# Kernel optimization log

Measured on AMD Instinct MI355X. Metric: run time of the kernel, lower is better.

## Reference

```python
import jax, jax.numpy as jnp
import numpy as np

R = 256        # residual channels
SKIP = 256     # skip channels
COND = 80      # conditioning (mel) channels
NUM_CLS = 256  # mu-law classes
T = 1024       # samples to generate
DILATIONS = tuple([1, 2, 4, 8, 16, 32, 64, 128, 256, 512] * 3)  # 30 layers, kernel_size=2
L = len(DILATIONS)


def setup_inputs() -> dict:
    key = jax.random.key(0)
    ks = jax.random.split(key, 15)
    sc = 0.05
    f = jnp.float32
    return {
        "y": jax.random.normal(ks[0], (COND, T), f),
        "emb": jnp.tanh(jax.random.normal(ks[1], (NUM_CLS, R), f)),  # buffer stores emb.tanh()
        "condition_W": jax.random.normal(ks[2], (L * 2 * R, COND), f) * sc,
        "WV_past": jax.random.normal(ks[3], (L, 2 * R, R), f) * sc,      # K=2 -> one past tap
        "WV_present": jax.random.normal(ks[4], (L, 2 * R, R), f) * sc,
        "W_o_weight": jax.random.normal(ks[5], (L - 1, R + SKIP, R), f) * sc,
        "W_o_bias": jax.random.normal(ks[6], (L - 1, R + SKIP), f) * sc,
        "W_o_weight_last": jax.random.normal(ks[7], (SKIP, R), f) * sc,
        "W_o_bias_last": jax.random.normal(ks[8], (SKIP,), f) * sc,
        "end1_w": jax.random.normal(ks[9], (SKIP, SKIP), f) * sc,
        "end1_b": jax.random.normal(ks[10], (SKIP,), f) * sc,
        "end2_w": jax.random.normal(ks[11], (NUM_CLS, SKIP), f) * sc,
        "end2_b": jax.random.normal(ks[12], (NUM_CLS,), f) * sc,
        "samples": jax.random.uniform(ks[13], (T,), f),  # torch.rand(T) inverse-CDF draws
    }


def _generate(y, emb, condition_W, WV_past, WV_present, W_o_weight, W_o_bias,
              W_o_weight_last, W_o_bias_last, end1_w, end1_b, end2_w, end2_b,
              samples, c=1.0):
    # all conditioning projections at once; chunked per layer as in torch.chunk(.., L, dim=0)
    conds_seq = (condition_W @ y).T.reshape(T, L, 2 * R)  # [T, L, 2R]
    x0 = emb[NUM_CLS // 2 - 1]
    mems0 = tuple(jnp.zeros((R, d), y.dtype) for d in DILATIONS)  # ring buffers per layer
    idx0 = jnp.zeros((L,), jnp.int32)

    def step(carry, inp):
        mems, idxs, x = carry
        cond_t, u = inp
        skip = jnp.zeros((SKIP,), x.dtype)
        new_mems, new_idxs = [], []
        for j in range(L):  # fixed small layer loop (structurally distinct buffers)
            mem, idx = mems[j], idxs[j]
            # kernel_size=2 -> single past tap read from ring buffer at idx
            h = cond_t[j] + WV_past[j] @ jnp.take(mem, idx, axis=1) + WV_present[j] @ x
            mem = mem.at[:, idx].set(x)  # write present sample, advance ring pointer
            new_mems.append(mem)
            new_idxs.append((idx + 1) % mem.shape[1])
            zw, zf = jnp.split(h, 2)
            z = jnp.tanh(zw) * jax.nn.sigmoid(zf)  # gated activation
            if j < L - 1:
                z2 = W_o_weight[j] @ z + W_o_bias[j]
                x = x + z2[:R]          # residual
                skip = skip + z2[R:]    # skip accumulation
            else:
                skip = skip + W_o_weight_last @ z + W_o_bias_last
        hid = jax.nn.relu(end1_w @ jax.nn.relu(skip) + end1_b)
        logits = (end2_w @ hid + end2_b) * c
        cum = jnp.cumsum(jax.nn.softmax(logits))
        new_idx = jnp.argmax(cum > u)  # first index with cum-prob > u  (inverse-CDF sample)
        return (tuple(new_mems), jnp.stack(new_idxs), emb[new_idx]), (new_idx, logits)

    _, (outputs, logits) = jax.lax.scan(step, (mems0, idx0, x0), (conds_seq, samples))
    return outputs.astype(jnp.int64), logits


def reference(y, emb, condition_W, WV_past, WV_present, W_o_weight, W_o_bias,
              W_o_weight_last, W_o_bias_last, end1_w, end1_b, end2_w, end2_b, samples):
    outputs, _ = _generate(y, emb, condition_W, WV_past, WV_present, W_o_weight,
                           W_o_bias, W_o_weight_last, W_o_bias_last,
                           end1_w, end1_b, end2_w, end2_b, samples)
    return outputs
```

## Files before the change

kernel.cpp:

```cpp
#include <hip/hip_runtime.h>
#include <stdint.h>


typedef unsigned long long u64;

#define TT 1024

#define OFF_PG   0
#define OFF_PS   (OFF_PG + 30*8*256*8)
#define OFF_XV   (OFF_PS + 30*8*256*8)
#define OFF_SB   (OFF_XV + 30*256*8)
#define OFF_HID  (OFF_SB + 30*256*8)
#define OFF_IDX  (OFF_HID + 256*8)
#define OFF_XH   (OFF_IDX + 64)
#define WS_NEED  ((size_t)OFF_XH + (size_t)30*1024*256*4)

__device__ __forceinline__ u64 ldp(const u64* p){
    return __hip_atomic_load((u64*)p, __ATOMIC_RELAXED, __HIP_MEMORY_SCOPE_AGENT);
}
__device__ __forceinline__ void stp(u64* p, float v, unsigned stamp){
    union { float f; unsigned u; } c; c.f = v;
    u64 w = ((u64)stamp << 32) | (u64)c.u;
    __hip_atomic_store(p, w, __ATOMIC_RELAXED, __HIP_MEMORY_SCOPE_AGENT);
}
__device__ __forceinline__ void stpu(u64* p, unsigned v, unsigned stamp){
    u64 w = ((u64)stamp << 32) | (u64)v;
    __hip_atomic_store(p, w, __ATOMIC_RELAXED, __HIP_MEMORY_SCOPE_AGENT);
}
__device__ __forceinline__ float pf(u64 w){
    union { unsigned u; float f; } c; c.u = (unsigned)(w & 0xffffffffu); return c.f;
}
__device__ __forceinline__ unsigned pstamp(u64 w){ return (unsigned)(w >> 32); }
__device__ __forceinline__ float ldf(const float* p){
    return __hip_atomic_load((float*)p, __ATOMIC_RELAXED, __HIP_MEMORY_SCOPE_AGENT);
}
__device__ __forceinline__ void stf(float* p, float v){
    __hip_atomic_store(p, v, __ATOMIC_RELAXED, __HIP_MEMORY_SCOPE_AGENT);
}
__device__ __forceinline__ long long rt(){
    return (long long)__builtin_amdgcn_s_memrealtime();
}
__device__ __forceinline__ void bar_lds(){
    asm volatile("s_waitcnt lgkmcnt(0)\n\ts_barrier" ::: "memory");
}

__global__ void __launch_bounds__(256, 1)
wavenet_v2(const float* __restrict__ gy,   const float* __restrict__ gemb,
           const float* __restrict__ gcw,  const float* __restrict__ gwvp,
           const float* __restrict__ gwvx, const float* __restrict__ gwo,
           const float* __restrict__ gwob, const float* __restrict__ gwol,
           const float* __restrict__ gwobl,const float* __restrict__ ge1w,
           const float* __restrict__ ge1b, const float* __restrict__ ge2w,
           const float* __restrict__ ge2b, const float* __restrict__ gsmp,
           float one, int* __restrict__ gout, char* __restrict__ ws)
{
    const int b = blockIdx.x, tid = threadIdx.x;
    const int xcd = b & 7, kk = b >> 3;
    const int jj = 4*xcd + (kk >> 3);
    const int cc = kk & 7;

    if (jj > 30 || (jj == 30 && cc > 2)) return;

    u64* PG   = (u64*)(ws + OFF_PG);
    u64* PS   = (u64*)(ws + OFF_PS);
    u64* XV   = (u64*)(ws + OFF_XV);
    u64* SB   = (u64*)(ws + OFF_SB);
    u64* HIDP = (u64*)(ws + OFF_HID);
    u64* IDXP = (u64*)(ws + OFF_IDX);
    float* xh = (float*)(ws + OFF_XH);

    __shared__ float sTap[256];
    __shared__ float sXin[256];
    __shared__ float sY[80];
    __shared__ float sZ[32];
    __shared__ float sred[8];
    __shared__ int   sidx[4];

    const long long ddl = rt() + 400000000LL;

    if (jj < 30){
        const int j   = jj;
        const int dil = 1 << (j % 10);
        const int q   = tid & 3;
        const int s   = (tid >> 2) & 15;
        const int w   = tid >> 6;
        const int gr  = (s < 8) ? (32*cc + 8*w + s)
                                : (256 + 32*cc + 8*w + (s - 8));

        const float* rw = (q < 2) ? (gwvp + ((size_t)j*512 + gr)*256 + 128*q)
                                  : (gwvx + ((size_t)j*512 + gr)*256 + 128*(q-2));
        float wv[128];
        #pragma unroll
        for (int i = 0; i < 32; i++){
            const int ci = (i + 2*q) & 31;
            wv[4*i+0] = rw[4*ci+0]*one; wv[4*i+1] = rw[4*ci+1]*one;
            wv[4*i+2] = rw[4*ci+2]*one; wv[4*i+3] = rw[4*ci+3]*one;
        }
        float cw[20];
        {
            const float* cp = gcw + ((size_t)(j*512 + gr))*80 + 20*q;
            #pragma unroll
            for (int i = 0; i < 20; i++) cw[i] = cp[i]*one;
        }
        float wo2[64]; float bres = 0.f, bskip = 0.f;
        if (j < 29){
            const float* w0 = gwo + ((size_t)j*512 + tid)*256 + 32*cc;
            const float* w1 = gwo + ((size_t)j*512 + 256 + tid)*256 + 32*cc;
            #pragma unroll
            for (int i = 0; i < 32; i++){ wo2[i] = w0[i]*one; wo2[32+i] = w1[i]*one; }
            bres  = gwob[j*512 + tid];
            bskip = gwob[j*512 + 256 + tid];
        } else {
            const float* w0 = gwol + (size_t)tid*256 + 32*cc;
            #pragma unroll
            for (int i = 0; i < 32; i++){ wo2[i] = w0[i]*one; wo2[32+i] = 0.f; }
            bskip = gwobl[tid];
        }

        u64* pgj = PG + (size_t)j*8*256;
        u64* psj = PS + (size_t)j*8*256;
        const u64* pgp = PG + (size_t)(j > 0 ? j-1 : 0)*8*256 + tid;
        const u64* psp = PS + (size_t)(j > 0 ? j-1 : 0)*8*256 + tid;
        const u64* xvp = XV + (size_t)(j > 0 ? j-1 : 0)*256 + tid;
        const u64* sbp = SB + (size_t)(j >= 2 ? j-1 : 0)*256 + tid;
        float* xhj = xh + (size_t)j*1024*256;
        float xv_prev = 0.f;

        for (int t = 0; t < TT; t++){
            const unsigned stamp = (unsigned)(t + 1);

            if (tid < 80) sY[tid] = gy[tid*TT + t];
            float tapv;
            if (dil == 1) tapv = xv_prev;
            else          tapv = (t >= dil) ? ldf(xhj + (size_t)(t-dil)*256 + tid) : 0.f;
            sTap[tid] = tapv;
            bar_lds();

            float acc = 0.f;
            #pragma unroll
            for (int i = 0; i < 20; i++) acc = fmaf(cw[i], sY[20*q + i], acc);
            if (q < 2){
                const float4* x4 = (const float4*)(sTap + 128*q);
                #pragma unroll
                for (int i = 0; i < 32; i++){
                    const int ci = (i + 2*q) & 31;
                    float4 v = x4[ci];
                    acc = fmaf(wv[4*i+0], v.x, acc); acc = fmaf(wv[4*i+1], v.y, acc);
                    acc = fmaf(wv[4*i+2], v.z, acc); acc = fmaf(wv[4*i+3], v.w, acc);
                }
            }

            float xv;
            if (j == 0){
                if (t == 0){
                    xv = gemb[127*256 + tid];
                } else {
                    u64 wIdx; int c = 0;
                    do {
                        wIdx = ldp(IDXP);
                        if (((++c) & 255) == 0 && rt() > ddl) break;
                    } while (pstamp(wIdx) != (unsigned)t);
                    const int idx = (int)(wIdx & 0xffffffffu) & 255;
                    xv = gemb[idx*256 + tid];
                }
            } else {
                u64 gwv[8]; u64 xvw = 0; u64 swv[8]; u64 sbw = 0;
                bool fresh; int c = 0;
                do {
                    #pragma unroll
                    for (int c2 = 0; c2 < 8; c2++) gwv[c2] = ldp(pgp + c2*256);
                    xvw = ldp(xvp);
                    bool ok = (pstamp(xvw) == stamp);
                    #pragma unroll
                    for (int c2 = 0; c2 < 8; c2++) ok &= (pstamp(gwv[c2]) == stamp);
                    if (cc == 0){
                        #pragma unroll
                        for (int c2 = 0; c2 < 8; c2++){
                            swv[c2] = ldp(psp + c2*256);
                            ok &= (pstamp(swv[c2]) == stamp);
                        }
                        if (j >= 2){ sbw = ldp(sbp); ok &= (pstamp(sbw) == stamp); }
                    }
                    fresh = ok;
                    if (((++c) & 255) == 0 && rt() > ddl) break;
                } while (!fresh);
                xv = pf(xvw);
                #pragma unroll
                for (int c2 = 0; c2 < 8; c2++) xv += pf(gwv[c2]);
                if (cc == 0){
                    float sv = (j >= 2) ? pf(sbw) : 0.f;
                    #pragma unroll
                    for (int c2 = 0; c2 < 8; c2++) sv += pf(swv[c2]);
                    stp(SB + (size_t)j*256 + tid, sv, stamp);
                }
            }
            xv_prev = xv;
            sXin[tid] = xv;
            if (cc == 0){
                stp(XV + (size_t)j*256 + tid, xv, stamp);
                if (dil > 1) stf(xhj + (size_t)t*256 + tid, xv);
            }
            bar_lds();

            if (q >= 2){
                const float4* x4 = (const float4*)(sXin + 128*(q-2));
                #pragma unroll
                for (int i = 0; i < 32; i++){
                    const int ci = (i + 2*q) & 31;
                    float4 v = x4[ci];
                    acc = fmaf(wv[4*i+0], v.x, acc); acc = fmaf(wv[4*i+1], v.y, acc);
                    acc = fmaf(wv[4*i+2], v.z, acc); acc = fmaf(wv[4*i+3], v.w, acc);
                }
            }
            acc += __shfl_xor(acc, 1, 64);
            acc += __shfl_xor(acc, 2, 64);
            const float hpart = __shfl_xor(acc, 32, 64);
            if (q == 0 && s < 8)
                sZ[8*w + s] = tanhf(acc) * (1.f/(1.f + expf(-hpart)));
            bar_lds();

            float g = 0.f, sk = 0.f;
            const float4* z4 = (const float4*)sZ;
            #pragma unroll
            for (int i = 0; i < 8; i++){
                float4 v = z4[i];
                g  = fmaf(wo2[4*i+0], v.x, g);  g  = fmaf(wo2[4*i+1], v.y, g);
                g  = fmaf(wo2[4*i+2], v.z, g);  g  = fmaf(wo2[4*i+3], v.w, g);
                sk = fmaf(wo2[32+4*i+0], v.x, sk); sk = fmaf(wo2[32+4*i+1], v.y, sk);
                sk = fmaf(wo2[32+4*i+2], v.z, sk); sk = fmaf(wo2[32+4*i+3], v.w, sk);
            }
            if (j < 29){
                if (cc == 0){ g += bres; sk += bskip; }
                stp(pgj + cc*256 + tid, g,  stamp);
                stp(psj + cc*256 + tid, sk, stamp);
            } else {
                if (cc == 0) g += bskip;
                stp(psj + cc*256 + tid, g, stamp);
            }
        }
        return;
    }

    if (jj == 30 && cc < 2){
        const int half = cc;
        const int r  = 128*half + (tid >> 1);
        const int hc = tid & 1;
        float e1[128];
        {
            const float* wp = ge1w + (size_t)r*256 + 128*hc;
            #pragma unroll
            for (int i = 0; i < 128; i++) e1[i] = wp[i]*one;
        }
        const float b1 = ge1b[r];
        const u64* psp = PS + (size_t)29*8*256 + tid;
        const u64* sbp = SB + (size_t)29*256 + tid;

        for (int t = 0; t < TT; t++){
            const unsigned stamp = (unsigned)(t + 1);
            u64 swv[8]; u64 sbw = 0; bool fresh; int c = 0;
            do {
                #pragma unroll
                for (int c2 = 0; c2 < 8; c2++) swv[c2] = ldp(psp + c2*256);
                sbw = ldp(sbp);
                bool ok = (pstamp(sbw) == stamp);
                #pragma unroll
                for (int c2 = 0; c2 < 8; c2++) ok &= (pstamp(swv[c2]) == stamp);
                fresh = ok;
                if (((++c) & 255) == 0 && rt() > ddl) break;
            } while (!fresh);
            float sk = pf(sbw);
            #pragma unroll
            for (int c2 = 0; c2 < 8; c2++) sk += pf(swv[c2]);
            sTap[tid] = fmaxf(sk, 0.f);
            bar_lds();
            float a = 0.f;
            const float4* p4 = (const float4*)(sTap + 128*hc);
            #pragma unroll
            for (int i = 0; i < 32; i++){
                float4 v = p4[i];
                a = fmaf(e1[4*i+0], v.x, a); a = fmaf(e1[4*i+1], v.y, a);
                a = fmaf(e1[4*i+2], v.z, a); a = fmaf(e1[4*i+3], v.w, a);
            }
            a += __shfl_xor(a, 1, 64);
            if (hc == 0) stp(HIDP + r, fmaxf(a + b1, 0.f), stamp);
            bar_lds();
        }
        return;
    }

    {
        float e2[256];
        {
            const float* wp = ge2w + (size_t)tid*256;
            #pragma unroll
            for (int i = 0; i < 256; i++) e2[i] = wp[i]*one;
        }
        const float b2 = ge2b[tid];
        const int w = tid >> 6, lane = tid & 63;

        for (int t = 0; t < TT; t++){
            const unsigned stamp = (unsigned)(t + 1);
            u64 hw; int c = 0;
            do {
                hw = ldp(HIDP + tid);
                if (((++c) & 255) == 0 && rt() > ddl) break;
            } while (pstamp(hw) != stamp);
            sTap[tid] = pf(hw);
            bar_lds();
            float a = b2;
            const float4* p4 = (const float4*)sTap;
            #pragma unroll
            for (int i = 0; i < 64; i++){
                float4 v = p4[i];
                a = fmaf(e2[4*i+0], v.x, a); a = fmaf(e2[4*i+1], v.y, a);
                a = fmaf(e2[4*i+2], v.z, a); a = fmaf(e2[4*i+3], v.w, a);
            }
            float m = a;
            #pragma unroll
            for (int off = 32; off > 0; off >>= 1) m = fmaxf(m, __shfl_xor(m, off, 64));
            if (lane == 0) sred[w] = m;
            bar_lds();
            m = fmaxf(fmaxf(sred[0], sred[1]), fmaxf(sred[2], sred[3]));
            float pe = expf(a - m);
            float ssum = pe;
            #pragma unroll
            for (int off = 32; off > 0; off >>= 1) ssum += __shfl_xor(ssum, off, 64);
            if (lane == 0) sred[4 + w] = ssum;
            bar_lds();
            const float S = sred[4] + sred[5] + sred[6] + sred[7];
            float cum = pe / S;
            #pragma unroll
            for (int off = 1; off < 64; off <<= 1){
                float vv = __shfl_up(cum, off, 64);
                if (lane >= off) cum += vv;
            }
            if (lane == 63) sred[w] = cum;
            bar_lds();
            float base = 0.f;
            if (w > 0) base += sred[0];
            if (w > 1) base += sred[1];
            if (w > 2) base += sred[2];
            cum += base;
            const float u = gsmp[t];
            unsigned long long bal = __ballot(cum > u);
            int cand = bal ? (w*64 + __ffsll((long long)bal) - 1) : (1 << 30);
            if (lane == 0) sidx[w] = cand;
            bar_lds();
            int idx = min(min(sidx[0], sidx[1]), min(sidx[2], sidx[3]));
            if (idx > 255) idx = 0;
            if (tid == 0){
                gout[t] = idx;
                stpu(IDXP, (unsigned)idx, stamp);
            }
            bar_lds();
        }
        return;
    }
}

__global__ void ws_too_small_kernel(int* out, int n){
    int i = blockIdx.x*256 + threadIdx.x;
    if (i < n) out[i] = 0;
}

extern "C" void kernel_launch(void* const* d_in, const int* in_sizes, int n_in,
                              void* d_out, int out_size, void* d_ws, size_t ws_size,
                              hipStream_t stream){
    (void)in_sizes; (void)n_in;
    if (ws_size < WS_NEED){
        hipLaunchKernelGGL(ws_too_small_kernel, dim3(4), dim3(256), 0, stream,
                           (int*)d_out, out_size);
        return;
    }
    hipLaunchKernelGGL(wavenet_v2, dim3(256), dim3(256), 0, stream,
                       (const float*)d_in[0],  (const float*)d_in[1],
                       (const float*)d_in[2],  (const float*)d_in[3],
                       (const float*)d_in[4],  (const float*)d_in[5],
                       (const float*)d_in[6],  (const float*)d_in[7],
                       (const float*)d_in[8],  (const float*)d_in[9],
                       (const float*)d_in[10], (const float*)d_in[11],
                       (const float*)d_in[12], (const float*)d_in[13],
                       1.0f, (int*)d_out, (char*)d_ws);
}
```

Before: 108.5 ms.

## Pack inter-layer flag records contiguously and move skip reduction to head block

Replaces the scattered per-chunk stamped buffers with one contiguous 128-byte record per layer row, holding the 8 gate partials plus xv, so a consumer polls it with five vector loads. The per-layer skip-sum chain through cc==0 blocks is removed. Skip partials go into a per-row array that the end1 block polls and sums directly over 30 layers. It also uses inline asm loads/stores with sc0 sc1 cache bypass and keeps weights in vector registers. This shortens the critical dependency chain between layers, at the cost of more polling work in the head block.

Result: slower. 195.2 ms (+79.8%).

```diff
diff --git a/kernel.cpp b/kernel.cpp
--- a/kernel.cpp
+++ b/kernel.cpp
@@ -3,68 +3,115 @@
 
 
 typedef unsigned long long u64;
+typedef float v16 __attribute__((ext_vector_type(16)));
 
 #define TT 1024
 
-#define OFF_PG   0
-#define OFF_PS   (OFF_PG + 30*8*256*8)
-#define OFF_XV   (OFF_PS + 30*8*256*8)
-#define OFF_SB   (OFF_XV + 30*256*8)
-#define OFF_HID  (OFF_SB + 30*256*8)
+#define OFF_REC  4096
+#define OFF_SPR  (OFF_REC + 29*256*128)
+#define OFF_HID  (OFF_SPR + 256*256*8)
 #define OFF_IDX  (OFF_HID + 256*8)
 #define OFF_XH   (OFF_IDX + 64)
 #define WS_NEED  ((size_t)OFF_XH + (size_t)30*1024*256*4)
 
-__device__ __forceinline__ u64 ldp(const u64* p){
-    return __hip_atomic_load((u64*)p, __ATOMIC_RELAXED, __HIP_MEMORY_SCOPE_AGENT);
-}
-__device__ __forceinline__ void stp(u64* p, float v, unsigned stamp){
+__device__ __forceinline__ long long rt(){
+    return (long long)__builtin_amdgcn_s_memrealtime();
+}
+__device__ __forceinline__ u64 pk(unsigned stamp, float v){
     union { float f; unsigned u; } c; c.f = v;
-    u64 w = ((u64)stamp << 32) | (u64)c.u;
-    __hip_atomic_store(p, w, __ATOMIC_RELAXED, __HIP_MEMORY_SCOPE_AGENT);
-}
-__device__ __forceinline__ void stpu(u64* p, unsigned v, unsigned stamp){
-    u64 w = ((u64)stamp << 32) | (u64)v;
-    __hip_atomic_store(p, w, __ATOMIC_RELAXED, __HIP_MEMORY_SCOPE_AGENT);
-}
-__device__ __forceinline__ float pf(u64 w){
-    union { unsigned u; float f; } c; c.u = (unsigned)(w & 0xffffffffu); return c.f;
-}
-__device__ __forceinline__ unsigned pstamp(u64 w){ return (unsigned)(w >> 32); }
+    return ((u64)stamp << 32) | (u64)c.u;
+}
+__device__ __forceinline__ u64 pku(unsigned stamp, unsigned v){
+    return ((u64)stamp << 32) | (u64)v;
+}
+__device__ __forceinline__ float uaf(unsigned u){
+    union { unsigned u; float f; } c; c.u = u; return c.f;
+}
+__device__ __forceinline__ unsigned pst(u64 w){ return (unsigned)(w >> 32); }
 __device__ __forceinline__ float ldf(const float* p){
     return __hip_atomic_load((float*)p, __ATOMIC_RELAXED, __HIP_MEMORY_SCOPE_AGENT);
 }
 __device__ __forceinline__ void stf(float* p, float v){
     __hip_atomic_store(p, v, __ATOMIC_RELAXED, __HIP_MEMORY_SCOPE_AGENT);
 }
-__device__ __forceinline__ long long rt(){
-    return (long long)__builtin_amdgcn_s_memrealtime();
+
+__device__ __forceinline__ u64 ld8_s(const void* p){
+    u64 r;
+    asm volatile("global_load_dwordx2 %0, %1, off sc0 sc1\n\ts_waitcnt vmcnt(0)"
+                 : "=&v"(r) : "v"(p) : "memory");
+    return r;
+}
+__device__ __forceinline__ void st8_s(void* p, u64 v){
+    asm volatile("global_store_dwordx2 %0, %1, off sc0 sc1" :: "v"(p), "v"(v) : "memory");
+}
+__device__ __forceinline__ void poll5_s(const void* p, uint4& a, uint4& b, uint4& c,
+                                        uint4& d, uint4& e){
+    asm volatile(
+        "global_load_dwordx4 %0, %5, off sc0 sc1\n\t"
+        "global_load_dwordx4 %1, %5, off offset:16 sc0 sc1\n\t"
+        "global_load_dwordx4 %2, %5, off offset:32 sc0 sc1\n\t"
+        "global_load_dwordx4 %3, %5, off offset:48 sc0 sc1\n\t"
+        "global_load_dwordx4 %4, %5, off offset:64 sc0 sc1\n\t"
+        "s_waitcnt vmcnt(0)"
+        : "=&v"(a),"=&v"(b),"=&v"(c),"=&v"(d),"=&v"(e) : "v"(p) : "memory");
+}
+__device__ __forceinline__ void poll4_s(const void* p, uint4& a, uint4& b, uint4& c,
+                                        uint4& d){
+    asm volatile(
+        "global_load_dwordx4 %0, %4, off sc0 sc1\n\t"
+        "global_load_dwordx4 %1, %4, off offset:16 sc0 sc1\n\t"
+        "global_load_dwordx4 %2, %4, off offset:32 sc0 sc1\n\t"
+        "global_load_dwordx4 %3, %4, off offset:48 sc0 sc1\n\t"
+        "s_waitcnt vmcnt(0)"
+        : "=&v"(a),"=&v"(b),"=&v"(c),"=&v"(d) : "v"(p) : "memory");
 }
 __device__ __forceinline__ void bar_lds(){
     asm volatile("s_waitcnt lgkmcnt(0)\n\ts_barrier" ::: "memory");
 }
 
+#define LD16(W, P) { \
+  W[0]=(P)[0]*one;  W[1]=(P)[1]*one;  W[2]=(P)[2]*one;  W[3]=(P)[3]*one;  \
+  W[4]=(P)[4]*one;  W[5]=(P)[5]*one;  W[6]=(P)[6]*one;  W[7]=(P)[7]*one;  \
+  W[8]=(P)[8]*one;  W[9]=(P)[9]*one;  W[10]=(P)[10]*one;W[11]=(P)[11]*one;\
+  W[12]=(P)[12]*one;W[13]=(P)[13]*one;W[14]=(P)[14]*one;W[15]=(P)[15]*one;\
+}
+
+#define MAT16(W, X4, C, ACC) { \
+  { float4 v_=(X4)[4*(C)+0]; ACC=fmaf(W[0],v_.x,ACC);  ACC=fmaf(W[1],v_.y,ACC);  ACC=fmaf(W[2],v_.z,ACC);  ACC=fmaf(W[3],v_.w,ACC); } \
+  { float4 v_=(X4)[4*(C)+1]; ACC=fmaf(W[4],v_.x,ACC);  ACC=fmaf(W[5],v_.y,ACC);  ACC=fmaf(W[6],v_.z,ACC);  ACC=fmaf(W[7],v_.w,ACC); } \
+  { float4 v_=(X4)[4*(C)+2]; ACC=fmaf(W[8],v_.x,ACC);  ACC=fmaf(W[9],v_.y,ACC);  ACC=fmaf(W[10],v_.z,ACC); ACC=fmaf(W[11],v_.w,ACC);} \
+  { float4 v_=(X4)[4*(C)+3]; ACC=fmaf(W[12],v_.x,ACC); ACC=fmaf(W[13],v_.y,ACC); ACC=fmaf(W[14],v_.z,ACC); ACC=fmaf(W[15],v_.w,ACC);} \
+}
+
+#define LDWV1(W, I, E) { const float* p_ = rw + 4*(((I)+twoq)&31); \
+  W[E+0]=p_[0]*one; W[E+1]=p_[1]*one; W[E+2]=p_[2]*one; W[E+3]=p_[3]*one; }
+#define LDWV(W, K) LDWV1(W,4*(K)+0,0) LDWV1(W,4*(K)+1,4) LDWV1(W,4*(K)+2,8) LDWV1(W,4*(K)+3,12)
+#define MATWV1(W, I, E, X4) { float4 v_=(X4)[(((I)+twoq)&31)]; \
+  acc=fmaf(W[E+0],v_.x,acc); acc=fmaf(W[E+1],v_.y,acc); acc=fmaf(W[E+2],v_.z,acc); acc=fmaf(W[E+3],v_.w,acc); }
+#define MATWV(W, K, X4) MATWV1(W,4*(K)+0,0,X4) MATWV1(W,4*(K)+1,4,X4) MATWV1(W,4*(K)+2,8,X4) MATWV1(W,4*(K)+3,12,X4)
+
+#define MATZ1(W, I, E, ACC) { float4 v_=z4[(I)]; \
+  ACC=fmaf(W[E+0],v_.x,ACC); ACC=fmaf(W[E+1],v_.y,ACC); ACC=fmaf(W[E+2],v_.z,ACC); ACC=fmaf(W[E+3],v_.w,ACC); }
+#define MATZ(W, IB, ACC) MATZ1(W,(IB)+0,0,ACC) MATZ1(W,(IB)+1,4,ACC) MATZ1(W,(IB)+2,8,ACC) MATZ1(W,(IB)+3,12,ACC)
+
 __global__ void __launch_bounds__(256, 1)
-wavenet_v2(const float* __restrict__ gy,   const float* __restrict__ gemb,
-           const float* __restrict__ gcw,  const float* __restrict__ gwvp,
-           const float* __restrict__ gwvx, const float* __restrict__ gwo,
-           const float* __restrict__ gwob, const float* __restrict__ gwol,
-           const float* __restrict__ gwobl,const float* __restrict__ ge1w,
-           const float* __restrict__ ge1b, const float* __restrict__ ge2w,
-           const float* __restrict__ ge2b, const float* __restrict__ gsmp,
-           float one, int* __restrict__ gout, char* __restrict__ ws)
+wavenet_v3c(const float* __restrict__ gy,   const float* __restrict__ gemb,
+            const float* __restrict__ gcw,  const float* __restrict__ gwvp,
+            const float* __restrict__ gwvx, const float* __restrict__ gwo,
+            const float* __restrict__ gwob, const float* __restrict__ gwol,
+            const float* __restrict__ gwobl,const float* __restrict__ ge1w,
+            const float* __restrict__ ge1b, const float* __restrict__ ge2w,
+            const float* __restrict__ ge2b, const float* __restrict__ gsmp,
+            float one, int* __restrict__ gout, char* __restrict__ ws)
 {
     const int b = blockIdx.x, tid = threadIdx.x;
-    const int xcd = b & 7, kk = b >> 3;
-    const int jj = 4*xcd + (kk >> 3);
+    const int xcdh = b & 7, kk = b >> 3;
+    const int jj = 4*xcdh + (kk >> 3);
     const int cc = kk & 7;
-
     if (jj > 30 || (jj == 30 && cc > 2)) return;
 
-    u64* PG   = (u64*)(ws + OFF_PG);
-    u64* PS   = (u64*)(ws + OFF_PS);
-    u64* XV   = (u64*)(ws + OFF_XV);
-    u64* SB   = (u64*)(ws + OFF_SB);
+    u64* REC  = (u64*)(ws + OFF_REC);
+    u64* SPR  = (u64*)(ws + OFF_SPR);
     u64* HIDP = (u64*)(ws + OFF_HID);
     u64* IDXP = (u64*)(ws + OFF_IDX);
     float* xh = (float*)(ws + OFF_XH);
@@ -84,45 +131,39 @@
         const int q   = tid & 3;
         const int s   = (tid >> 2) & 15;
         const int w   = tid >> 6;
-        const int gr  = (s < 8) ? (32*cc + 8*w + s)
-                                : (256 + 32*cc + 8*w + (s - 8));
+        const int twoq = 2*q;
+        const int gr  = (s < 8) ? (32*cc + 8*w + s) : (256 + 32*cc + 8*w + (s - 8));
 
         const float* rw = (q < 2) ? (gwvp + ((size_t)j*512 + gr)*256 + 128*q)
                                   : (gwvx + ((size_t)j*512 + gr)*256 + 128*(q-2));
-        float wv[128];
-        #pragma unroll
-        for (int i = 0; i < 32; i++){
-            const int ci = (i + 2*q) & 31;
-            wv[4*i+0] = rw[4*ci+0]*one; wv[4*i+1] = rw[4*ci+1]*one;
-            wv[4*i+2] = rw[4*ci+2]*one; wv[4*i+3] = rw[4*ci+3]*one;
-        }
-        float cw[20];
+        v16 wv0,wv1,wv2,wv3,wv4,wv5,wv6,wv7;
+        LDWV(wv0,0) LDWV(wv1,1) LDWV(wv2,2) LDWV(wv3,3)
+        LDWV(wv4,4) LDWV(wv5,5) LDWV(wv6,6) LDWV(wv7,7)
+
+        v16 cwa; float4 cwb;
         {
             const float* cp = gcw + ((size_t)(j*512 + gr))*80 + 20*q;
-            #pragma unroll
-            for (int i = 0; i < 20; i++) cw[i] = cp[i]*one;
-        }
-        float wo2[64]; float bres = 0.f, bskip = 0.f;
+            LD16(cwa, cp);
+            cwb.x = cp[16]*one; cwb.y = cp[17]*one; cwb.z = cp[18]*one; cwb.w = cp[19]*one;
+        }
+        const float* w0 = (j < 29) ? (gwo + ((size_t)j*512 + tid)*256 + 32*cc)
+                                   : (gwol + (size_t)tid*256 + 32*cc);
+        v16 wg0, wg1;
+        LD16(wg0, w0); LD16(wg1, w0+16);
+        v16 ws0, ws1;
+        float bres = 0.f, bskip;
         if (j < 29){
-            const float* w0 = gwo + ((size_t)j*512 + tid)*256 + 32*cc;
             const float* w1 = gwo + ((size_t)j*512 + 256 + tid)*256 + 32*cc;
-            #pragma unroll
-            for (int i = 0; i < 32; i++){ wo2[i] = w0[i]*one; wo2[32+i] = w1[i]*one; }
+            LD16(ws0, w1); LD16(ws1, w1+16);
             bres  = gwob[j*512 + tid];
             bskip = gwob[j*512 + 256 + tid];
         } else {
-            const float* w0 = gwol + (size_t)tid*256 + 32*cc;
-            #pragma unroll
-            for (int i = 0; i < 32; i++){ wo2[i] = w0[i]*one; wo2[32+i] = 0.f; }
             bskip = gwobl[tid];
         }
 
-        u64* pgj = PG + (size_t)j*8*256;
-        u64* psj = PS + (size_t)j*8*256;
-        const u64* pgp = PG + (size_t)(j > 0 ? j-1 : 0)*8*256 + tid;
-        const u64* psp = PS + (size_t)(j > 0 ? j-1 : 0)*8*256 + tid;
-        const u64* xvp = XV + (size_t)(j > 0 ? j-1 : 0)*256 + tid;
-        const u64* sbp = SB + (size_t)(j >= 2 ? j-1 : 0)*256 + tid;
+        u64* growp = REC + ((size_t)j*256 + tid)*16;
+        const char* pollb = (const char*)(REC + ((size_t)(j>0?j-1:0)*256 + tid)*16);
+        u64* sprow = SPR + (size_t)tid*256 + (size_t)j*8 + cc;
         float* xhj = xh + (size_t)j*1024*256;
         float xv_prev = 0.f;
 
@@ -137,17 +178,23 @@
             bar_lds();
 
             float acc = 0.f;
-            #pragma unroll
-            for (int i = 0; i < 20; i++) acc = fmaf(cw[i], sY[20*q + i], acc);
+            {
+                const float* yb = sY + 20*q;
+                acc=fmaf(cwa[0],yb[0],acc);   acc=fmaf(cwa[1],yb[1],acc);
+                acc=fmaf(cwa[2],yb[2],acc);   acc=fmaf(cwa[3],yb[3],acc);
+                acc=fmaf(cwa[4],yb[4],acc);   acc=fmaf(cwa[5],yb[5],acc);
+                acc=fmaf(cwa[6],yb[6],acc);   acc=fmaf(cwa[7],yb[7],acc);
+                acc=fmaf(cwa[8],yb[8],acc);   acc=fmaf(cwa[9],yb[9],acc);
+                acc=fmaf(cwa[10],yb[10],acc); acc=fmaf(cwa[11],yb[11],acc);
+                acc=fmaf(cwa[12],yb[12],acc); acc=fmaf(cwa[13],yb[13],acc);
+                acc=fmaf(cwa[14],yb[14],acc); acc=fmaf(cwa[15],yb[15],acc);
+                acc=fmaf(cwb.x,yb[16],acc);   acc=fmaf(cwb.y,yb[17],acc);
+                acc=fmaf(cwb.z,yb[18],acc);   acc=fmaf(cwb.w,yb[19],acc);
+            }
             if (q < 2){
-                const float4* x4 = (const float4*)(sTap + 128*q);
-                #pragma unroll
-                for (int i = 0; i < 32; i++){
-                    const int ci = (i + 2*q) & 31;
-                    float4 v = x4[ci];
-                    acc = fmaf(wv[4*i+0], v.x, acc); acc = fmaf(wv[4*i+1], v.y, acc);
-                    acc = fmaf(wv[4*i+2], v.z, acc); acc = fmaf(wv[4*i+3], v.w, acc);
-                }
+                const float4* x4p = (const float4*)(sTap + 128*q);
+                MATWV(wv0,0,x4p) MATWV(wv1,1,x4p) MATWV(wv2,2,x4p) MATWV(wv3,3,x4p)
+                MATWV(wv4,4,x4p) MATWV(wv5,5,x4p) MATWV(wv6,6,x4p) MATWV(wv7,7,x4p)
             }
 
             float xv;
@@ -157,60 +204,39 @@
                 } else {
                     u64 wIdx; int c = 0;
                     do {
-                        wIdx = ldp(IDXP);
+                        wIdx = ld8_s(IDXP);
                         if (((++c) & 255) == 0 && rt() > ddl) break;
-                    } while (pstamp(wIdx) != (unsigned)t);
+                    } while (pst(wIdx) != (unsigned)t);
                     const int idx = (int)(wIdx & 0xffffffffu) & 255;
                     xv = gemb[idx*256 + tid];
                 }
             } else {
-                u64 gwv[8]; u64 xvw = 0; u64 swv[8]; u64 sbw = 0;
-                bool fresh; int c = 0;
+                uint4 r0,r1,r2v,r3v,r4v; bool ok; int c = 0;
                 do {
-                    #pragma unroll
-                    for (int c2 = 0; c2 < 8; c2++) gwv[c2] = ldp(pgp + c2*256);
-                    xvw = ldp(xvp);
-                    bool ok = (pstamp(xvw) == stamp);
-                    #pragma unroll
-                    for (int c2 = 0; c2 < 8; c2++) ok &= (pstamp(gwv[c2]) == stamp);
-                    if (cc == 0){
-                        #pragma unroll
-                        for (int c2 = 0; c2 < 8; c2++){
-                            swv[c2] = ldp(psp + c2*256);
-                            ok &= (pstamp(swv[c2]) == stamp);
-                        }
-                        if (j >= 2){ sbw = ldp(sbp); ok &= (pstamp(sbw) == stamp); }
-                    }
-                    fresh = ok;
+                    poll5_s(pollb, r0,r1,r2v,r3v,r4v);
+                    ok = (r0.y==stamp) & (r0.w==stamp) & (r1.y==stamp) & (r1.w==stamp)
+                       & (r2v.y==stamp) & (r2v.w==stamp) & (r3v.y==stamp) & (r3v.w==stamp)
+                       & (r4v.y==stamp);
                     if (((++c) & 255) == 0 && rt() > ddl) break;
-                } while (!fresh);
-                xv = pf(xvw);
-                #pragma unroll
-                for (int c2 = 0; c2 < 8; c2++) xv += pf(gwv[c2]);
-                if (cc == 0){
-                    float sv = (j >= 2) ? pf(sbw) : 0.f;
-                    #pragma unroll
-                    for (int c2 = 0; c2 < 8; c2++) sv += pf(swv[c2]);
-                    stp(SB + (size_t)j*256 + tid, sv, stamp);
-                }
+                } while (!ok);
+                xv  = uaf(r4v.x);
+                xv += uaf(r0.x);  xv += uaf(r0.z);
+                xv += uaf(r1.x);  xv += uaf(r1.z);
+                xv += uaf(r2v.x); xv += uaf(r2v.z);
+                xv += uaf(r3v.x); xv += uaf(r3v.z);
             }
             xv_prev = xv;
             sXin[tid] = xv;
             if (cc == 0){
-                stp(XV + (size_t)j*256 + tid, xv, stamp);
-                if (dil > 1) stf(xhj + (size_t)t*256 + tid, xv);
+                if (j <= 28) st8_s(growp + 8, pk(stamp, xv));
+                if (dil > 1) stf(&xhj[(size_t)t*256 + tid], xv);
             }
             bar_lds();
 
             if (q >= 2){
-                const float4* x4 = (const float4*)(sXin + 128*(q-2));
-                #pragma unroll
-                for (int i = 0; i < 32; i++){
-                    const int ci = (i + 2*q) & 31;
-                    float4 v = x4[ci];
-                    acc = fmaf(wv[4*i+0], v.x, acc); acc = fmaf(wv[4*i+1], v.y, acc);
-                    acc = fmaf(wv[4*i+2], v.z, acc); acc = fmaf(wv[4*i+3], v.w, acc);
-                }
+                const float4* x4p = (const float4*)(sXin + 128*(q-2));
+                MATWV(wv0,0,x4p) MATWV(wv1,1,x4p) MATWV(wv2,2,x4p) MATWV(wv3,3,x4p)
+                MATWV(wv4,4,x4p) MATWV(wv5,5,x4p) MATWV(wv6,6,x4p) MATWV(wv7,7,x4p)
             }
             acc += __shfl_xor(acc, 1, 64);
             acc += __shfl_xor(acc, 2, 64);
@@ -219,23 +245,19 @@
                 sZ[8*w + s] = tanhf(acc) * (1.f/(1.f + expf(-hpart)));
             bar_lds();
 
-            float g = 0.f, sk = 0.f;
             const float4* z4 = (const float4*)sZ;
-            #pragma unroll
-            for (int i = 0; i < 8; i++){
-                float4 v = z4[i];
-                g  = fmaf(wo2[4*i+0], v.x, g);  g  = fmaf(wo2[4*i+1], v.y, g);
-                g  = fmaf(wo2[4*i+2], v.z, g);  g  = fmaf(wo2[4*i+3], v.w, g);
-                sk = fmaf(wo2[32+4*i+0], v.x, sk); sk = fmaf(wo2[32+4*i+1], v.y, sk);
-                sk = fmaf(wo2[32+4*i+2], v.z, sk); sk = fmaf(wo2[32+4*i+3], v.w, sk);
-            }
             if (j < 29){
+                float g = 0.f, sk = 0.f;
+                MATZ(wg0, 0, g)  MATZ(wg1, 4, g)
+                MATZ(ws0, 0, sk) MATZ(ws1, 4, sk)
                 if (cc == 0){ g += bres; sk += bskip; }
-                stp(pgj + cc*256 + tid, g,  stamp);
-                stp(psj + cc*256 + tid, sk, stamp);
+                st8_s(growp + cc, pk(stamp, g));
+                st8_s(sprow, pk(stamp, sk));
             } else {
+                float g = 0.f;
+                MATZ(wg0, 0, g) MATZ(wg1, 4, g)
                 if (cc == 0) g += bskip;
-                stp(psj + cc*256 + tid, g, stamp);
+                st8_s(sprow, pk(stamp, g));
             }
         }
         return;
@@ -245,56 +267,50 @@
         const int half = cc;
         const int r  = 128*half + (tid >> 1);
         const int hc = tid & 1;
-        float e1[128];
-        {
-            const float* wp = ge1w + (size_t)r*256 + 128*hc;
-            #pragma unroll
-            for (int i = 0; i < 128; i++) e1[i] = wp[i]*one;
-        }
+        const float* wp = ge1w + (size_t)r*256 + 128*hc;
+        v16 e0,e1v,e2v,e3,e4,e5,e6,e7;
+        LD16(e0,wp);    LD16(e1v,wp+16); LD16(e2v,wp+32); LD16(e3,wp+48);
+        LD16(e4,wp+64); LD16(e5,wp+80);  LD16(e6,wp+96);  LD16(e7,wp+112);
         const float b1 = ge1b[r];
-        const u64* psp = PS + (size_t)29*8*256 + tid;
-        const u64* sbp = SB + (size_t)29*256 + tid;
+        const u64* sprb = SPR + (size_t)tid*256;
 
         for (int t = 0; t < TT; t++){
             const unsigned stamp = (unsigned)(t + 1);
-            u64 swv[8]; u64 sbw = 0; bool fresh; int c = 0;
-            do {
-                #pragma unroll
-                for (int c2 = 0; c2 < 8; c2++) swv[c2] = ldp(psp + c2*256);
-                sbw = ldp(sbp);
-                bool ok = (pstamp(sbw) == stamp);
-                #pragma unroll
-                for (int c2 = 0; c2 < 8; c2++) ok &= (pstamp(swv[c2]) == stamp);
-                fresh = ok;
-                if (((++c) & 255) == 0 && rt() > ddl) break;
-            } while (!fresh);
-            float sk = pf(sbw);
-            #pragma unroll
-            for (int c2 = 0; c2 < 8; c2++) sk += pf(swv[c2]);
+            float sk = 0.f;
+            for (int l = 0; l < 30; l++){
+                uint4 r0,r1,r2v,r3v; bool ok; int c = 0;
+                const void* p = (const void*)(sprb + l*8);
+                do {
+                    poll4_s(p, r0,r1,r2v,r3v);
+                    ok = (r0.y==stamp)&(r0.w==stamp)&(r1.y==stamp)&(r1.w==stamp)
+                       & (r2v.y==stamp)&(r2v.w==stamp)&(r3v.y==stamp)&(r3v.w==stamp);
+                    if (((++c) & 255) == 0 && rt() > ddl) break;
+                } while (!ok);
+                sk += uaf(r0.x);  sk += uaf(r0.z);
+                sk += uaf(r1.x);  sk += uaf(r1.z);
+                sk += uaf(r2v.x); sk += uaf(r2v.z);
+                sk += uaf(r3v.x); sk += uaf(r3v.z);
+            }
             sTap[tid] = fmaxf(sk, 0.f);
             bar_lds();
             float a = 0.f;
             const float4* p4 = (const float4*)(sTap + 128*hc);
-            #pragma unroll
-            for (int i = 0; i < 32; i++){
-                float4 v = p4[i];
-                a = fmaf(e1[4*i+0], v.x, a); a = fmaf(e1[4*i+1], v.y, a);
-                a = fmaf(e1[4*i+2], v.z, a); a = fmaf(e1[4*i+3], v.w, a);
-            }
+            MAT16(e0,p4,0,a)  MAT16(e1v,p4,1,a) MAT16(e2v,p4,2,a) MAT16(e3,p4,3,a)
+            MAT16(e4,p4,4,a)  MAT16(e5,p4,5,a)  MAT16(e6,p4,6,a)  MAT16(e7,p4,7,a)
             a += __shfl_xor(a, 1, 64);
-            if (hc == 0) stp(HIDP + r, fmaxf(a + b1, 0.f), stamp);
+            if (hc == 0) st8_s(HIDP + r, pk(stamp, fmaxf(a + b1, 0.f)));
             bar_lds();
         }
         return;
     }
 
     {
-        float e2[256];
-        {
-            const float* wp = ge2w + (size_t)tid*256;
-            #pragma unroll
-            for (int i = 0; i < 256; i++) e2[i] = wp[i]*one;
-        }
+        const float* wp = ge2w + (size_t)tid*256;
+        v16 f0,f1,f2,f3,f4,f5,f6,f7,f8,f9,fa,fb,fc,fd,fe,ff;
+        LD16(f0,wp);     LD16(f1,wp+16);  LD16(f2,wp+32);  LD16(f3,wp+48);
+        LD16(f4,wp+64);  LD16(f5,wp+80);  LD16(f6,wp+96);  LD16(f7,wp+112);
+        LD16(f8,wp+128); LD16(f9,wp+144); LD16(fa,wp+160); LD16(fb,wp+176);
+        LD16(fc,wp+192); LD16(fd,wp+208); LD16(fe,wp+224); LD16(ff,wp+240);
         const float b2 = ge2b[tid];
         const int w = tid >> 6, lane = tid & 63;
 
@@ -302,19 +318,17 @@
             const unsigned stamp = (unsigned)(t + 1);
             u64 hw; int c = 0;
             do {
-                hw = ldp(HIDP + tid);
+                hw = ld8_s(HIDP + tid);
                 if (((++c) & 255) == 0 && rt() > ddl) break;
-            } while (pstamp(hw) != stamp);
-            sTap[tid] = pf(hw);
+            } while (pst(hw) != stamp);
+            sTap[tid] = uaf((unsigned)(hw & 0xffffffffu));
             bar_lds();
             float a = b2;
             const float4* p4 = (const float4*)sTap;
-            #pragma unroll
-            for (int i = 0; i < 64; i++){
-                float4 v = p4[i];
-                a = fmaf(e2[4*i+0], v.x, a); a = fmaf(e2[4*i+1], v.y, a);
-                a = fmaf(e2[4*i+2], v.z, a); a = fmaf(e2[4*i+3], v.w, a);
-            }
+            MAT16(f0,p4,0,a)  MAT16(f1,p4,1,a)  MAT16(f2,p4,2,a)  MAT16(f3,p4,3,a)
+            MAT16(f4,p4,4,a)  MAT16(f5,p4,5,a)  MAT16(f6,p4,6,a)  MAT16(f7,p4,7,a)
+            MAT16(f8,p4,8,a)  MAT16(f9,p4,9,a)  MAT16(fa,p4,10,a) MAT16(fb,p4,11,a)
+            MAT16(fc,p4,12,a) MAT16(fd,p4,13,a) MAT16(fe,p4,14,a) MAT16(ff,p4,15,a)
             float m = a;
             #pragma unroll
             for (int off = 32; off > 0; off >>= 1) m = fmaxf(m, __shfl_xor(m, off, 64));
@@ -350,7 +364,7 @@
             if (idx > 255) idx = 0;
             if (tid == 0){
                 gout[t] = idx;
-                stpu(IDXP, (unsigned)idx, stamp);
+                st8_s(IDXP, pku(stamp, (unsigned)idx));
             }
             bar_lds();
         }
@@ -372,7 +386,7 @@
                            (int*)d_out, out_size);
         return;
     }
-    hipLaunchKernelGGL(wavenet_v2, dim3(256), dim3(256), 0, stream,
+    hipLaunchKernelGGL(wavenet_v3c, dim3(256), dim3(256), 0, stream,
                        (const float*)d_in[0],  (const float*)d_in[1],
                        (const float*)d_in[2],  (const float*)d_in[3],
                        (const float*)d_in[4],  (const float*)d_in[5],
```
